# Kernel tuning notes

Measured on AMD Instinct MI355X. Metric: run time of the kernel, lower is better.

## Reference

```python
import jax, jax.numpy as jnp
import numpy as np

E, C, M, H, O = 8, 4096, 1024, 4096, 1024

def setup_inputs() -> dict:
    key = jax.random.key(0)
    k = jax.random.split(key, 5)
    # kaiming-uniform-ish scales (exact init distribution not needed for correctness baseline)
    s1 = 1.0 / np.sqrt(M)
    s2 = 1.0 / np.sqrt(H)
    return {
        'x': jax.random.normal(k[0], (E, C, M), dtype=jnp.float32),
        'fc1_w': jax.random.uniform(k[1], (E, H, M), minval=-s1, maxval=s1, dtype=jnp.float32),
        'fc1_b': jax.random.uniform(k[2], (E, H), minval=-s1, maxval=s1, dtype=jnp.float32),
        'fc2_w': jax.random.uniform(k[3], (E, H, O), minval=-s2, maxval=s2, dtype=jnp.float32),
        'fc2_b': jax.random.uniform(k[4], (E, O), minval=-s2, maxval=s2, dtype=jnp.float32),
    }

def reference(x, fc1_w, fc1_b, fc2_w, fc2_b):
    # y = relu(x @ fc1_w^T + b1) @ fc2_w + b2, batched over experts e
    h = jnp.einsum('ecm,ehm->ech', x, fc1_w) + fc1_b[:, None, :]
    h = jax.nn.relu(h)
    y = jnp.einsum('ech,eho->eco', h, fc2_w) + fc2_b[:, None, :]
    return y
```

## Files before the change

### kernel.cpp

```cpp
#include <hip/hip_runtime.h>


typedef __bf16 bf16x8 __attribute__((ext_vector_type(8)));
typedef float f32x4 __attribute__((ext_vector_type(4)));

__device__ __forceinline__ unsigned short f2bf(float f) {
  union { float f; unsigned int u; } v; v.f = f;
  unsigned int u = v.u;
  u += 0x7fffu + ((u >> 16) & 1u);
  return (unsigned short)(u >> 16);
}

#define GLD_LDS16(gptr, lptr)                                               \
  __builtin_amdgcn_global_load_lds(                                         \
      (const __attribute__((address_space(1))) void*)(gptr),                \
      (__attribute__((address_space(3))) void*)(lptr), 16, 0, 0)

__global__ void cvt_bf16_kernel(const float* __restrict__ in,
                                unsigned short* __restrict__ out, long n) {
  long i = ((long)blockIdx.x * blockDim.x + threadIdx.x) * 4;
  if (i >= n) return;
  const float4 v = *(const float4*)(in + i);
  ushort4 o;
  o.x = f2bf(v.x); o.y = f2bf(v.y); o.z = f2bf(v.z); o.w = f2bf(v.w);
  *(ushort4*)(out + i) = o;
}

__global__ void transpose_cvt_kernel(const float* __restrict__ in,
                                     unsigned short* __restrict__ out,
                                     int H, int O, long istride, long ostride) {
  __shared__ unsigned short tile[32][33];
  const float* inp = in + (long)blockIdx.z * istride;
  unsigned short* outp = out + (long)blockIdx.z * ostride;
  const int o0 = blockIdx.x * 32, h0 = blockIdx.y * 32;
  const int tx = threadIdx.x, ty = threadIdx.y;
#pragma unroll
  for (int r = ty; r < 32; r += 8)
    tile[r][tx] = f2bf(inp[(long)(h0 + r) * O + o0 + tx]);
  __syncthreads();
#pragma unroll
  for (int r = ty; r < 32; r += 8)
    outp[(long)(o0 + r) * H + h0 + tx] = tile[tx][r];
}

#define BM 128
#define BN 128
#define BK 64

template <int EPI>
__global__ __launch_bounds__(256) void gemm_bt_kernel(
    const unsigned short* __restrict__ A, const unsigned short* __restrict__ B,
    const float* __restrict__ bias, void* __restrict__ Cout,
    int Nd, int Kd, long sA, long sB, long sBias, long sC) {
  __shared__ unsigned short As[BM * BK];
  __shared__ unsigned short Bs[BN * BK];

  const int e = blockIdx.z;
  const unsigned short* Ae = A + (long)e * sA;
  const unsigned short* Be = B + (long)e * sB;
  const float* be = bias + (long)e * sBias;

  const int tid = threadIdx.x;
  const int wave = tid >> 6;
  const int lane = tid & 63;

  const int blockM = blockIdx.y * BM;
  const int blockN = blockIdx.x * BN;

  const int srow = lane >> 3;
  const int skc = ((lane & 7) ^ srow) * 8;
  const unsigned short* gA = Ae + (long)(blockM + srow) * Kd + skc;
  const unsigned short* gB = Be + (long)(blockN + srow) * Kd + skc;

  const int wm = wave >> 1;
  const int wn = wave & 1;
  const int fr = lane & 15;
  const int quad = lane >> 4;
  const int fsw = fr & 7;

  f32x4 acc[4][4];
#pragma unroll
  for (int a = 0; a < 4; ++a)
#pragma unroll
    for (int b = 0; b < 4; ++b) acc[a][b] = (f32x4){0.f, 0.f, 0.f, 0.f};

  for (int k0 = 0; k0 < Kd; k0 += BK) {
    __syncthreads();
#pragma unroll
    for (int i = 0; i < 4; ++i) {
      const int c = wave * 4 + i;
      GLD_LDS16(gA + (long)(c * 8) * Kd + k0, &As[c * 512]);
      GLD_LDS16(gB + (long)(c * 8) * Kd + k0, &Bs[c * 512]);
    }
    __syncthreads();
#pragma unroll
    for (int kk = 0; kk < BK; kk += 32) {
      const int slot = ((quad + (kk >> 3)) ^ fsw) * 8;
      bf16x8 af[4], bfr[4];
#pragma unroll
      for (int mi = 0; mi < 4; ++mi)
        af[mi] = *(const bf16x8*)&As[(wm * 64 + mi * 16 + fr) * BK + slot];
#pragma unroll
      for (int ni = 0; ni < 4; ++ni)
        bfr[ni] = *(const bf16x8*)&Bs[(wn * 64 + ni * 16 + fr) * BK + slot];
#pragma unroll
      for (int mi = 0; mi < 4; ++mi)
#pragma unroll
        for (int ni = 0; ni < 4; ++ni)
          acc[mi][ni] = __builtin_amdgcn_mfma_f32_16x16x32_bf16(
              af[mi], bfr[ni], acc[mi][ni], 0, 0, 0);
    }
  }

  float bv[4];
#pragma unroll
  for (int ni = 0; ni < 4; ++ni) bv[ni] = be[blockN + wn * 64 + ni * 16 + fr];

  if (EPI == 0) {
    unsigned short* Co = (unsigned short*)Cout + (long)e * sC;
#pragma unroll
    for (int mi = 0; mi < 4; ++mi) {
      const int m = blockM + wm * 64 + mi * 16 + quad * 4;
#pragma unroll
      for (int r = 0; r < 4; ++r) {
        const long rowoff = (long)(m + r) * Nd;
#pragma unroll
        for (int ni = 0; ni < 4; ++ni) {
          float v = acc[mi][ni][r] + bv[ni];
          v = v > 0.f ? v : 0.f;
          Co[rowoff + blockN + wn * 64 + ni * 16 + fr] = f2bf(v);
        }
      }
    }
  } else {
    float* Co = (float*)Cout + (long)e * sC;
#pragma unroll
    for (int mi = 0; mi < 4; ++mi) {
      const int m = blockM + wm * 64 + mi * 16 + quad * 4;
#pragma unroll
      for (int r = 0; r < 4; ++r) {
        const long rowoff = (long)(m + r) * Nd;
#pragma unroll
        for (int ni = 0; ni < 4; ++ni)
          Co[rowoff + blockN + wn * 64 + ni * 16 + fr] = acc[mi][ni][r] + bv[ni];
      }
    }
  }
}

extern "C" void kernel_launch(void* const* d_in, const int* in_sizes, int n_in,
                              void* d_out, int out_size, void* d_ws,
                              size_t ws_size, hipStream_t stream) {
  const float* x  = (const float*)d_in[0];
  const float* w1 = (const float*)d_in[1];
  const float* b1 = (const float*)d_in[2];
  const float* w2 = (const float*)d_in[3];
  const float* b2 = (const float*)d_in[4];
  float* out = (float*)d_out;

  const int E = 8, C = 4096, M = 1024, H = 4096, O = 1024;
  const long nx  = (long)C * M;
  const long nw1 = (long)H * M;
  const long nw2 = (long)O * H;
  const long nh  = (long)C * H;

  unsigned short* ws = (unsigned short*)d_ws;
  const size_t needBatch = (size_t)(E * (nx + nw1 + nw2 + nh)) * 2;

  if (ws_size >= needBatch) {
    unsigned short* xb  = ws;
    unsigned short* w1b = xb + E * nx;
    unsigned short* w2t = w1b + E * nw1;
    unsigned short* hb  = w2t + E * nw2;
    const long tx = E * nx, tw1 = E * nw1;
    cvt_bf16_kernel<<<tx / 1024, 256, 0, stream>>>(x, xb, tx);
    cvt_bf16_kernel<<<tw1 / 1024, 256, 0, stream>>>(w1, w1b, tw1);
    transpose_cvt_kernel<<<dim3(O / 32, H / 32, E), dim3(32, 8), 0, stream>>>(
        w2, w2t, H, O, (long)H * O, (long)O * H);
    gemm_bt_kernel<0><<<dim3(H / BN, C / BM, E), 256, 0, stream>>>(
        xb, w1b, b1, hb, H, M, nx, nw1, H, nh);
    gemm_bt_kernel<1><<<dim3(O / BN, C / BM, E), 256, 0, stream>>>(
        hb, w2t, b2, out, O, H, nh, nw2, O, (long)C * O);
  } else {
    unsigned short* xb  = ws;
    unsigned short* w1b = xb + nx;
    unsigned short* w2t = w1b + nw1;
    unsigned short* hb  = w2t + nw2;
    for (int e = 0; e < E; ++e) {
      cvt_bf16_kernel<<<nx / 1024, 256, 0, stream>>>(x + e * nx, xb, nx);
      cvt_bf16_kernel<<<nw1 / 1024, 256, 0, stream>>>(w1 + e * nw1, w1b, nw1);
      transpose_cvt_kernel<<<dim3(O / 32, H / 32, 1), dim3(32, 8), 0, stream>>>(
          w2 + e * nw2, w2t, H, O, 0, 0);
      gemm_bt_kernel<0><<<dim3(H / BN, C / BM, 1), 256, 0, stream>>>(
          xb, w1b, b1 + (long)e * H, hb, H, M, 0, 0, 0, 0);
      gemm_bt_kernel<1><<<dim3(O / BN, C / BM, 1), 256, 0, stream>>>(
          hb, w2t, b2 + (long)e * O, out + e * nx, O, H, 0, 0, 0, 0);
    }
  }
}
```

Baseline: 1.071 ms.

## Enlarge GEMM tiles to 256x256 with double-buffered LDS ping-pong pipeline

Each GEMM block now covers a 256x256 tile using 512 threads (8 waves). LDS is double-buffered, and each K step is split into four MFMA phases that interleave the direct global-to-LDS loads for the next tile, using barriers, vmcnt waits and s_setprio. The block id is remapped to spread consecutive workgroups across XCDs. The aim is to hide global load latency and raise data reuse per tile, at the cost of more registers and LDS per block, fewer blocks in the grid, and fragile hand-tuned synchronisation.

```diff
diff --git a/kernel.cpp b/kernel.cpp
--- a/kernel.cpp
+++ b/kernel.cpp
@@ -43,73 +43,159 @@
     outp[(long)(o0 + r) * H + h0 + tx] = tile[tx][r];
 }
 
-#define BM 128
-#define BN 128
+#define BM 256
+#define BN 256
 #define BK 64
 
 template <int EPI>
-__global__ __launch_bounds__(256) void gemm_bt_kernel(
+__global__ __launch_bounds__(512, 2) void gemm_bt_kernel(
     const unsigned short* __restrict__ A, const unsigned short* __restrict__ B,
     const float* __restrict__ bias, void* __restrict__ Cout,
     int Nd, int Kd, long sA, long sB, long sBias, long sC) {
-  __shared__ unsigned short As[BM * BK];
-  __shared__ unsigned short Bs[BN * BK];
-
-  const int e = blockIdx.z;
-  const unsigned short* Ae = A + (long)e * sA;
-  const unsigned short* Be = B + (long)e * sB;
-  const float* be = bias + (long)e * sBias;
+  __shared__ unsigned short As[2][BM * BK];
+  __shared__ unsigned short Bs[2][BN * BK];
+
+  const int nbx = gridDim.x;
+  const int nbxy = nbx * gridDim.y;
+  const int nwg = nbxy * gridDim.z;
+  int gid = blockIdx.x + nbx * blockIdx.y + nbxy * blockIdx.z;
+  gid = (gid & 7) * (nwg >> 3) + (gid >> 3);
+  const int bz = gid / nbxy;
+  const int rem = gid - bz * nbxy;
+  const int by = rem / nbx;
+  const int bx = rem - by * nbx;
+
+  const unsigned short* Ae = A + (long)bz * sA;
+  const unsigned short* Be = B + (long)bz * sB;
+  const float* be = bias + (long)bz * sBias;
 
   const int tid = threadIdx.x;
   const int wave = tid >> 6;
   const int lane = tid & 63;
-
-  const int blockM = blockIdx.y * BM;
-  const int blockN = blockIdx.x * BN;
-
-  const int srow = lane >> 3;
-  const int skc = ((lane & 7) ^ srow) * 8;
-  const unsigned short* gA = Ae + (long)(blockM + srow) * Kd + skc;
-  const unsigned short* gB = Be + (long)(blockN + srow) * Kd + skc;
-
-  const int wm = wave >> 1;
-  const int wn = wave & 1;
+  const int wm = wave >> 2;
+  const int wn = wave & 3;
   const int fr = lane & 15;
   const int quad = lane >> 4;
   const int fsw = fr & 7;
 
-  f32x4 acc[4][4];
-#pragma unroll
-  for (int a = 0; a < 4; ++a)
+  const int blockM = by * BM;
+  const int blockN = bx * BN;
+
+  const int srow = tid >> 3;
+  const int skc = ((tid & 7) ^ (srow & 7)) * 8;
+  const unsigned short* gA = Ae + (long)(blockM + srow) * Kd + skc;
+  const unsigned short* gB = Be + (long)(blockN + srow) * Kd + skc;
+
+#define STAGE_A(buf, band, kt)                                              \
+  GLD_LDS16(gA + (long)(band) * Kd + (kt) * BK,                             \
+            &As[buf][(band) * BK + wave * 512])
+#define STAGE_B(buf, band, kt)                                              \
+  GLD_LDS16(gB + (long)(band) * Kd + (kt) * BK,                             \
+            &Bs[buf][(band) * BK + wave * 512])
+#define STAGE_A_MH0(buf, kt) { STAGE_A(buf, 0, kt);   STAGE_A(buf, 128, kt); }
+#define STAGE_A_MH1(buf, kt) { STAGE_A(buf, 64, kt);  STAGE_A(buf, 192, kt); }
+#define STAGE_B_R0(buf, kt)  { STAGE_B(buf, 0, kt);   STAGE_B(buf, 64, kt);  }
+#define STAGE_B_R1(buf, kt)  { STAGE_B(buf, 128, kt); STAGE_B(buf, 192, kt); }
+#define VMWAIT4 asm volatile("s_waitcnt vmcnt(4)" ::: "memory")
+
+  f32x4 acc[8][4];
+#pragma unroll
+  for (int a = 0; a < 8; ++a)
 #pragma unroll
     for (int b = 0; b < 4; ++b) acc[a][b] = (f32x4){0.f, 0.f, 0.f, 0.f};
 
-  for (int k0 = 0; k0 < Kd; k0 += BK) {
-    __syncthreads();
-#pragma unroll
-    for (int i = 0; i < 4; ++i) {
-      const int c = wave * 4 + i;
-      GLD_LDS16(gA + (long)(c * 8) * Kd + k0, &As[c * 512]);
-      GLD_LDS16(gB + (long)(c * 8) * Kd + k0, &Bs[c * 512]);
-    }
-    __syncthreads();
-#pragma unroll
-    for (int kk = 0; kk < BK; kk += 32) {
-      const int slot = ((quad + (kk >> 3)) ^ fsw) * 8;
-      bf16x8 af[4], bfr[4];
-#pragma unroll
-      for (int mi = 0; mi < 4; ++mi)
-        af[mi] = *(const bf16x8*)&As[(wm * 64 + mi * 16 + fr) * BK + slot];
-#pragma unroll
-      for (int ni = 0; ni < 4; ++ni)
-        bfr[ni] = *(const bf16x8*)&Bs[(wn * 64 + ni * 16 + fr) * BK + slot];
-#pragma unroll
-      for (int mi = 0; mi < 4; ++mi)
-#pragma unroll
-        for (int ni = 0; ni < 4; ++ni)
-          acc[mi][ni] = __builtin_amdgcn_mfma_f32_16x16x32_bf16(
-              af[mi], bfr[ni], acc[mi][ni], 0, 0, 0);
-    }
+  const int NT = Kd / BK;
+
+  const int aRow = (wm * 128 + fr) * BK;
+  const int bRow = (wn * 64 + fr) * BK;
+  const int s0 = (quad ^ fsw) * 8;
+  const int s1 = ((4 + quad) ^ fsw) * 8;
+
+  STAGE_B_R0(0, 0);
+  STAGE_A_MH0(0, 0);
+  STAGE_B_R1(0, 0);
+  STAGE_A_MH1(0, 0);
+  STAGE_B_R0(1, (NT > 1 ? 1 : 0));
+  VMWAIT4;
+  __builtin_amdgcn_s_barrier();
+
+  bf16x8 af[4], bfr[4];
+
+  for (int t = 0; t < NT; ++t) {
+    const int cur = t & 1;
+    const int nxt = cur ^ 1;
+    const int k1 = (t + 1 < NT) ? t + 1 : NT - 1;
+    const int k2 = (t + 2 < NT) ? t + 2 : NT - 1;
+    const unsigned short* Asc = &As[cur][0];
+    const unsigned short* Bsc = &Bs[cur][0];
+
+#pragma unroll
+    for (int ni = 0; ni < 4; ++ni)
+      bfr[ni] = *(const bf16x8*)&Bsc[bRow + ni * 16 * BK + s0];
+#pragma unroll
+    for (int i = 0; i < 4; ++i)
+      af[i] = *(const bf16x8*)&Asc[aRow + i * 16 * BK + s0];
+    STAGE_A_MH0(nxt, k1);
+    __builtin_amdgcn_s_barrier();
+    __builtin_amdgcn_s_setprio(1);
+#pragma unroll
+    for (int i = 0; i < 4; ++i)
+#pragma unroll
+      for (int ni = 0; ni < 4; ++ni)
+        acc[i][ni] = __builtin_amdgcn_mfma_f32_16x16x32_bf16(
+            af[i], bfr[ni], acc[i][ni], 0, 0, 0);
+    __builtin_amdgcn_s_setprio(0);
+    VMWAIT4;
+    __builtin_amdgcn_s_barrier();
+
+#pragma unroll
+    for (int i = 0; i < 4; ++i)
+      af[i] = *(const bf16x8*)&Asc[aRow + (64 + i * 16) * BK + s0];
+    STAGE_B_R1(nxt, k1);
+    __builtin_amdgcn_s_barrier();
+    __builtin_amdgcn_s_setprio(1);
+#pragma unroll
+    for (int i = 0; i < 4; ++i)
+#pragma unroll
+      for (int ni = 0; ni < 4; ++ni)
+        acc[4 + i][ni] = __builtin_amdgcn_mfma_f32_16x16x32_bf16(
+            af[i], bfr[ni], acc[4 + i][ni], 0, 0, 0);
+    __builtin_amdgcn_s_setprio(0);
+    __builtin_amdgcn_s_barrier();
+
+#pragma unroll
+    for (int ni = 0; ni < 4; ++ni)
+      bfr[ni] = *(const bf16x8*)&Bsc[bRow + ni * 16 * BK + s1];
+#pragma unroll
+    for (int i = 0; i < 4; ++i)
+      af[i] = *(const bf16x8*)&Asc[aRow + i * 16 * BK + s1];
+    STAGE_A_MH1(nxt, k1);
+    __builtin_amdgcn_s_barrier();
+    __builtin_amdgcn_s_setprio(1);
+#pragma unroll
+    for (int i = 0; i < 4; ++i)
+#pragma unroll
+      for (int ni = 0; ni < 4; ++ni)
+        acc[i][ni] = __builtin_amdgcn_mfma_f32_16x16x32_bf16(
+            af[i], bfr[ni], acc[i][ni], 0, 0, 0);
+    __builtin_amdgcn_s_setprio(0);
+    __builtin_amdgcn_s_barrier();
+
+#pragma unroll
+    for (int i = 0; i < 4; ++i)
+      af[i] = *(const bf16x8*)&Asc[aRow + (64 + i * 16) * BK + s1];
+    STAGE_B_R0(cur, k2);
+    __builtin_amdgcn_s_barrier();
+    __builtin_amdgcn_s_setprio(1);
+#pragma unroll
+    for (int i = 0; i < 4; ++i)
+#pragma unroll
+      for (int ni = 0; ni < 4; ++ni)
+        acc[4 + i][ni] = __builtin_amdgcn_mfma_f32_16x16x32_bf16(
+            af[i], bfr[ni], acc[4 + i][ni], 0, 0, 0);
+    __builtin_amdgcn_s_setprio(0);
+    VMWAIT4;
+    __builtin_amdgcn_s_barrier();
   }
 
   float bv[4];
@@ -117,10 +203,10 @@
   for (int ni = 0; ni < 4; ++ni) bv[ni] = be[blockN + wn * 64 + ni * 16 + fr];
 
   if (EPI == 0) {
-    unsigned short* Co = (unsigned short*)Cout + (long)e * sC;
-#pragma unroll
-    for (int mi = 0; mi < 4; ++mi) {
-      const int m = blockM + wm * 64 + mi * 16 + quad * 4;
+    unsigned short* Co = (unsigned short*)Cout + (long)bz * sC;
+#pragma unroll
+    for (int mi = 0; mi < 8; ++mi) {
+      const int m = blockM + wm * 128 + mi * 16 + quad * 4;
 #pragma unroll
       for (int r = 0; r < 4; ++r) {
         const long rowoff = (long)(m + r) * Nd;
@@ -133,10 +219,10 @@
       }
     }
   } else {
-    float* Co = (float*)Cout + (long)e * sC;
-#pragma unroll
-    for (int mi = 0; mi < 4; ++mi) {
-      const int m = blockM + wm * 64 + mi * 16 + quad * 4;
+    float* Co = (float*)Cout + (long)bz * sC;
+#pragma unroll
+    for (int mi = 0; mi < 8; ++mi) {
+      const int m = blockM + wm * 128 + mi * 16 + quad * 4;
 #pragma unroll
       for (int r = 0; r < 4; ++r) {
         const long rowoff = (long)(m + r) * Nd;
@@ -177,9 +263,9 @@
     cvt_bf16_kernel<<<tw1 / 1024, 256, 0, stream>>>(w1, w1b, tw1);
     transpose_cvt_kernel<<<dim3(O / 32, H / 32, E), dim3(32, 8), 0, stream>>>(
         w2, w2t, H, O, (long)H * O, (long)O * H);
-    gemm_bt_kernel<0><<<dim3(H / BN, C / BM, E), 256, 0, stream>>>(
+    gemm_bt_kernel<0><<<dim3(H / BN, C / BM, E), 512, 0, stream>>>(
         xb, w1b, b1, hb, H, M, nx, nw1, H, nh);
-    gemm_bt_kernel<1><<<dim3(O / BN, C / BM, E), 256, 0, stream>>>(
+    gemm_bt_kernel<1><<<dim3(O / BN, C / BM, E), 512, 0, stream>>>(
         hb, w2t, b2, out, O, H, nh, nw2, O, (long)C * O);
   } else {
     unsigned short* xb  = ws;
@@ -191,9 +277,9 @@
       cvt_bf16_kernel<<<nw1 / 1024, 256, 0, stream>>>(w1 + e * nw1, w1b, nw1);
       transpose_cvt_kernel<<<dim3(O / 32, H / 32, 1), dim3(32, 8), 0, stream>>>(
           w2 + e * nw2, w2t, H, O, 0, 0);
-      gemm_bt_kernel<0><<<dim3(H / BN, C / BM, 1), 256, 0, stream>>>(
+      gemm_bt_kernel<0><<<dim3(H / BN, C / BM, 1), 512, 0, stream>>>(
           xb, w1b, b1 + (long)e * H, hb, H, M, 0, 0, 0, 0);
-      gemm_bt_kernel<1><<<dim3(O / BN, C / BM, 1), 256, 0, stream>>>(
+      gemm_bt_kernel<1><<<dim3(O / BN, C / BM, 1), 512, 0, stream>>>(
           hb, w2t, b2 + (long)e * O, out + e * nx, O, H, 0, 0, 0, 0);
     }
   }
```

New measurement: 1.150 ms. +7.3%, slower.
